# Performance work log

Measured on AMD Instinct MI355X. Metric: run time of the kernel, lower is better.

Reference implementation:

```python
import jax, jax.numpy as jnp
import numpy as np

MAX_ITERS = 30
NDIM = 3
TAU = 1.0 / (2.0 * NDIM)  # skimage Chambolle step size


def _grad(u, ax):
    # forward difference along ax, zero at the last slice (skimage convention)
    g = jnp.diff(u, axis=ax)
    pad = [(0, 0)] * u.ndim
    pad[ax] = (0, 1)
    return jnp.pad(g, pad)


def _div(p):
    # adjoint of _grad: d[ax] = shift_forward(p[ax]) - p[ax]
    d = jnp.zeros_like(p[0])
    for ax in range(NDIM):
        pa = p[ax]
        sl = [slice(None)] * NDIM
        sl[ax] = slice(0, -1)
        pad = [(0, 0)] * NDIM
        pad[ax] = (1, 0)
        d = d + jnp.pad(pa[tuple(sl)], pad) - pa
    return d


def tv_chambolle_nd(image, weight):
    # Chambolle projection algorithm (skimage _denoise_tv_chambolle_nd), fixed iters.
    def step(p, _):
        out = image + _div(p)
        g = jnp.stack([_grad(out, ax) for ax in range(NDIM)], axis=0)  # (3,B,T,F)
        norm = jnp.sqrt(jnp.sum(g * g, axis=0, keepdims=True))
        norm = norm * (TAU / weight) + 1.0
        return (p - TAU * g) / norm, None

    p0 = jnp.zeros((NDIM,) + image.shape, image.dtype)
    # iteration i returns out built from p after i updates; after max_iters loop
    # iterations the returned `out` used p updated (max_iters-1) times.
    p, _ = jax.lax.scan(jax.checkpoint(step), p0, None, length=MAX_ITERS - 1)
    return image + _div(p)


def setup_inputs() -> dict:
    key = jax.random.key(0)
    kx, kl, kb = jax.random.split(key, 3)
    x = jax.random.normal(kx, (8, 2048, 128), dtype=jnp.float32)
    # lambdas has a non-neg constraint; keep it strictly positive
    lambdas = jax.random.uniform(kl, (1, 1), dtype=jnp.float32) * 0.1 + 0.05
    b = jax.random.normal(kb, (1, 1, 128), dtype=jnp.float32) * 0.01
    return {"x": x, "lambdas": lambdas, "b": b}


def reference(x, lambdas, b):
    out = tv_chambolle_nd(x.astype(jnp.float32), lambdas)
    out = out + b  # use_bias=True; activation=None
    return out
```

## Files before the change

### kernel.cpp

```cpp
#include <hip/hip_runtime.h>
#include <hip/hip_fp16.h>


#define BB 8
#define TT 2048
#define FF 128
#define NV (BB*TT*FF)
#define SB (TT*FF)
#define ST FF
#define RR 8
#define NBLK (TT/RR)
#define HH 4
#define EE 16
#define GR 8

constexpr float TAU = 1.0f / 6.0f;

__device__ __forceinline__ float4 ld4(const float* p) { return *reinterpret_cast<const float4*>(p); }
__device__ __forceinline__ void st4(float* p, const float4& v) { *reinterpret_cast<float4*>(p) = v; }
__device__ __forceinline__ float4 ld4h(const __half* p) {
    uint2 u = *reinterpret_cast<const uint2*>(p);
    __half2 h0 = *reinterpret_cast<__half2*>(&u.x);
    __half2 h1 = *reinterpret_cast<__half2*>(&u.y);
    float2 a = __half22float2(h0), b2 = __half22float2(h1);
    return make_float4(a.x, a.y, b2.x, b2.y);
}
__device__ __forceinline__ void st4h(__half* p, const float4& v) {
    __half2 h0 = __float22half2_rn(make_float2(v.x, v.y));
    __half2 h1 = __float22half2_rn(make_float2(v.z, v.w));
    uint2 u;
    u.x = *reinterpret_cast<unsigned*>(&h0);
    u.y = *reinterpret_cast<unsigned*>(&h1);
    *reinterpret_cast<uint2*>(p) = u;
}
__device__ __forceinline__ float dpp_shr1(float v) {
    return __int_as_float(__builtin_amdgcn_update_dpp(
        0, __float_as_int(v), 0x111, 0xF, 0xF, true));
}
__device__ __forceinline__ float dpp_shl1(float v) {
    return __int_as_float(__builtin_amdgcn_update_dpp(
        0, __float_as_int(v), 0x101, 0xF, 0xF, true));
}
__device__ __forceinline__ float4 dpp_up4(const float4& v) {
    return make_float4(dpp_shr1(v.x), dpp_shr1(v.y), dpp_shr1(v.z), dpp_shr1(v.w));
}
__device__ __forceinline__ float4 dpp_dn4(const float4& v) {
    return make_float4(dpp_shl1(v.x), dpp_shl1(v.y), dpp_shl1(v.z), dpp_shl1(v.w));
}
__device__ __forceinline__ float4 sub4(const float4& a, const float4& b) {
    return make_float4(a.x - b.x, a.y - b.y, a.z - b.z, a.w - b.w);
}
__device__ __forceinline__ float4 f4z() { return make_float4(0.f, 0.f, 0.f, 0.f); }
__device__ __forceinline__ float4 nbvec(const float4& gB, const float4& gT, const float4& gF, float s) {
    float4 nb; float q;
    q = gB.x * gB.x + gT.x * gT.x + gF.x * gF.x;
    nb.x = __builtin_amdgcn_rcpf(fmaf(__builtin_amdgcn_sqrtf(q), s, 1.f));
    q = gB.y * gB.y + gT.y * gT.y + gF.y * gF.y;
    nb.y = __builtin_amdgcn_rcpf(fmaf(__builtin_amdgcn_sqrtf(q), s, 1.f));
    q = gB.z * gB.z + gT.z * gT.z + gF.z * gF.z;
    nb.z = __builtin_amdgcn_rcpf(fmaf(__builtin_amdgcn_sqrtf(q), s, 1.f));
    q = gB.w * gB.w + gT.w * gT.w + gF.w * gF.w;
    nb.w = __builtin_amdgcn_rcpf(fmaf(__builtin_amdgcn_sqrtf(q), s, 1.f));
    return nb;
}

struct ConeShared {
    float p2b[EE][4][8];
    float outx[EE][4][8];
    float4 p1if[256];
    float4 oif[256];
};

template<int RG>
__device__ __forceinline__ void publish(int k, float4 (&P1)[GR], float4 (&P2)[GR],
                                        ConeShared& sh, int c, int b, int fg, int w) {
    if (fg == 7) {
        #pragma unroll
        for (int le = 0; le < GR; ++le) {
            const int e = RG * GR + le;
            if (e >= k && e < EE - k) sh.p2b[e][w][b] = P2[le].w;
        }
    }
    if (RG == 0) sh.p1if[c] = P1[GR - 1];
}

template<int RG, bool ELO, bool EHI>
__device__ __forceinline__ void phase_out(
    int k, const float4 (&Xr)[GR],
    float4 (&P0)[GR], float4 (&P1)[GR], float4 (&P2)[GR], float4 (&O)[GR],
    ConeShared& sh, int c, int b, int fg, int w, int f0, int tb) {
    #pragma unroll
    for (int le = 0; le < GR; ++le) {
        const int e = RG * GR + le;
        if (e < k + 1 || e >= EE - k) continue;
        const int t = tb + e;
        if ((ELO && t < 0) || (EHI && t >= TT)) continue;
        const float4 X = Xr[le];
        float4 o;
        o.x = X.x - P0[le].x - P1[le].x - P2[le].x;
        o.y = X.y - P0[le].y - P1[le].y - P2[le].y + P2[le].x;
        o.z = X.z - P0[le].z - P1[le].z - P2[le].z + P2[le].y;
        o.w = X.w - P0[le].w - P1[le].w - P2[le].w + P2[le].z;
        float4 h0 = dpp_up4(P0[le]);
        if (b > 0) { o.x += h0.x; o.y += h0.y; o.z += h0.z; o.w += h0.w; }
        float4 pm1 = (le > 0) ? P1[le - 1] : sh.p1if[c];
        if (!ELO || t > 0) { o.x += pm1.x; o.y += pm1.y; o.z += pm1.z; o.w += pm1.w; }
        float pw = __shfl_up(P2[le].w, 8);
        if (fg == 0) pw = (w > 0) ? sh.p2b[e][(w - 1)][b] : 0.0f;
        if (f0 > 0) o.x += pw;
        O[le] = o;
        if (fg == 0) sh.outx[e][w][b] = o.x;
    }
}

template<int RG, bool ELO, bool EHI>
__device__ __forceinline__ void phase_upd(
    int k, float4 (&P0)[GR], float4 (&P1)[GR], float4 (&P2)[GR], float4 (&O)[GR],
    ConeShared& sh, int c, int b, int fg, int w, int f0, int tb, float s) {
    #pragma unroll
    for (int le = 0; le < GR; ++le) {
        const int e = RG * GR + le;
        if (e < k + 1 || e > EE - 2 - k) continue;
        const int t = tb + e;
        if ((ELO && t < 0) || (EHI && t >= TT)) continue;
        const float4 cc = O[le];
        const float4 on = (le < GR - 1) ? O[le + 1] : sh.oif[c];
        float4 gT = f4z();
        if (!EHI || t < TT - 1) gT = sub4(on, cc);
        const float4 nB = dpp_dn4(cc);
        float4 gB = f4z();
        if (b < BB - 1) gB = sub4(nB, cc);
        float nxx = __shfl_down(cc.x, 8);
        if (fg == 7) nxx = (w < 3) ? sh.outx[e][w + 1][b] : 0.0f;
        float4 gF;
        gF.x = cc.y - cc.x;
        gF.y = cc.z - cc.y;
        gF.z = cc.w - cc.z;
        gF.w = (f0 < FF - 4) ? (nxx - cc.w) : 0.f;
        const float4 nb = nbvec(gB, gT, gF, s);
        P0[le].x = fmaf(-TAU, gB.x, P0[le].x) * nb.x;
        P0[le].y = fmaf(-TAU, gB.y, P0[le].y) * nb.y;
        P0[le].z = fmaf(-TAU, gB.z, P0[le].z) * nb.z;
        P0[le].w = fmaf(-TAU, gB.w, P0[le].w) * nb.w;
        P1[le].x = fmaf(-TAU, gT.x, P1[le].x) * nb.x;
        P1[le].y = fmaf(-TAU, gT.y, P1[le].y) * nb.y;
        P1[le].z = fmaf(-TAU, gT.z, P1[le].z) * nb.z;
        P1[le].w = fmaf(-TAU, gT.w, P1[le].w) * nb.w;
        P2[le].x = fmaf(-TAU, gF.x, P2[le].x) * nb.x;
        P2[le].y = fmaf(-TAU, gF.y, P2[le].y) * nb.y;
        P2[le].z = fmaf(-TAU, gF.z, P2[le].z) * nb.z;
        P2[le].w = fmaf(-TAU, gF.w, P2[le].w) * nb.w;
    }
}

template<bool ELO, bool EHI>
__device__ __forceinline__ void cone_run(
    const float4 (&Xr)[GR],
    float4 (&P0)[GR], float4 (&P1)[GR], float4 (&P2)[GR], float4 (&O)[GR],
    ConeShared& sh, int rg, int c, int b, int fg, int w, int f0, int tb, float s) {
    #pragma unroll
    for (int k = 0; k < HH; ++k) {
        if (rg == 0) publish<0>(k, P1, P2, sh, c, b, fg, w);
        else         publish<1>(k, P1, P2, sh, c, b, fg, w);
        __syncthreads();
        if (rg == 0) phase_out<0, ELO, EHI>(k, Xr, P0, P1, P2, O, sh, c, b, fg, w, f0, tb);
        else         phase_out<1, ELO, EHI>(k, Xr, P0, P1, P2, O, sh, c, b, fg, w, f0, tb);
        if (rg == 1) sh.oif[c] = O[0];
        __syncthreads();
        if (rg == 0) phase_upd<0, ELO, EHI>(k, P0, P1, P2, O, sh, c, b, fg, w, f0, tb, s);
        else         phase_upd<1, ELO, EHI>(k, P0, P1, P2, O, sh, c, b, fg, w, f0, tb, s);
    }
}

template<bool ELO, bool EHI>
__device__ __forceinline__ void mid_main(
    const float* __restrict__ x, const __half* __restrict__ pin, __half* __restrict__ pout,
    ConeShared& sh, int rg, int c, int b, int fg, int w, int f0, int tb, int e0,
    int base, float s) {
    float4 P0[GR], P1[GR], P2[GR], O[GR], Xr[GR];
    #pragma unroll
    for (int le = 0; le < GR; ++le) {
        const int t = tb + e0 + le;
        const bool ok = (!ELO || t >= 0) && (!EHI || t < TT);
        const bool trim = (rg == 0 && le == 0);
        if (ok) {
            const int v = base + t * ST;
            P1[le] = ld4h(pin + NV + v);
            if (!trim) {
                P0[le] = ld4h(pin + v);
                P2[le] = ld4h(pin + 2 * NV + v);
                Xr[le] = ld4(x + v);
            } else { P0[le] = f4z(); P2[le] = f4z(); Xr[le] = f4z(); }
        } else {
            P0[le] = f4z(); P1[le] = f4z(); P2[le] = f4z(); Xr[le] = f4z();
        }
        O[le] = f4z();
    }
    cone_run<ELO, EHI>(Xr, P0, P1, P2, O, sh, rg, c, b, fg, w, f0, tb, s);
    #pragma unroll
    for (int le = 0; le < GR; ++le) {
        const int e = e0 + le;
        if (e >= HH && e < HH + RR) {
            const int v = base + (tb + e) * ST;
            st4h(pout + v, P0[le]);
            st4h(pout + NV + v, P1[le]);
            st4h(pout + 2 * NV + v, P2[le]);
        }
    }
}

__global__ __launch_bounds__(512, 2)
void k_mid(const float* __restrict__ x, const __half* __restrict__ pin,
           __half* __restrict__ pout, const float* __restrict__ lam) {
    __shared__ ConeShared sh;
    const int tid = threadIdx.x;
    const int blk = blockIdx.x;
    const int rg  = tid >> 8;
    const int c   = tid & 255;
    const int b   = tid & 7;
    const int fg  = (tid >> 3) & 7;
    const int w   = (tid >> 6) & 3;
    const int f0  = w * 32 + fg * 4;
    const int tb  = blk * RR - HH;
    const int e0  = rg * GR;
    const int base = b * SB + f0;
    const float s = TAU / lam[0];
    if (blk == 0 || blk == NBLK - 1)
        mid_main<true, true>(x, pin, pout, sh, rg, c, b, fg, w, f0, tb, e0, base, s);
    else
        mid_main<false, false>(x, pin, pout, sh, rg, c, b, fg, w, f0, tb, e0, base, s);
}

template<bool ELO, bool EHI>
__device__ __forceinline__ void first_main(
    const float* __restrict__ x, __half* __restrict__ pout,
    ConeShared& sh, int rg, int c, int b, int fg, int w, int f0, int tb, int e0,
    int base, float s) {
    float4 P0[GR], P1[GR], P2[GR], O[GR], Xr[GR], XHa;
    #pragma unroll
    for (int le = 0; le < GR; ++le) {
        const int t = tb + e0 + le;
        const bool ok = (!ELO || t >= 0) && (!EHI || t < TT);
        Xr[le] = ok ? ld4(x + base + t * ST) : f4z();
        O[le] = f4z();
    }
    {
        const int t = tb + e0 + GR;
        const bool ok = (!ELO || t >= 0) && (t < TT);
        XHa = ok ? ld4(x + base + t * ST) : f4z();
    }
    #pragma unroll
    for (int le = 0; le < GR; ++le) {
        const int t = tb + e0 + le;
        if ((!ELO || t >= 0) && (!EHI || t < TT)) {
            const float4 cc = Xr[le];
            const float4 nxt = (le < GR - 1) ? Xr[le + 1] : XHa;
            float4 gT = f4z();
            if (t < TT - 1) gT = sub4(nxt, cc);
            const float4 nB = dpp_dn4(cc);
            float4 gB = f4z();
            if (b < BB - 1) gB = sub4(nB, cc);
            float4 gF;
            gF.x = cc.y - cc.x;
            gF.y = cc.z - cc.y;
            gF.z = cc.w - cc.z;
            gF.w = (f0 < FF - 4) ? (x[base + t * ST + 4] - cc.w) : 0.f;
            const float4 nb = nbvec(gB, gT, gF, s);
            P0[le] = make_float4(-TAU * gB.x * nb.x, -TAU * gB.y * nb.y,
                                 -TAU * gB.z * nb.z, -TAU * gB.w * nb.w);
            P1[le] = make_float4(-TAU * gT.x * nb.x, -TAU * gT.y * nb.y,
                                 -TAU * gT.z * nb.z, -TAU * gT.w * nb.w);
            P2[le] = make_float4(-TAU * gF.x * nb.x, -TAU * gF.y * nb.y,
                                 -TAU * gF.z * nb.z, -TAU * gF.w * nb.w);
        } else {
            P0[le] = f4z(); P1[le] = f4z(); P2[le] = f4z();
        }
    }
    cone_run<ELO, EHI>(Xr, P0, P1, P2, O, sh, rg, c, b, fg, w, f0, tb, s);
    #pragma unroll
    for (int le = 0; le < GR; ++le) {
        const int e = e0 + le;
        if (e >= HH && e < HH + RR) {
            const int v = base + (tb + e) * ST;
            st4h(pout + v, P0[le]);
            st4h(pout + NV + v, P1[le]);
            st4h(pout + 2 * NV + v, P2[le]);
        }
    }
}

__global__ __launch_bounds__(512, 2)
void k_first(const float* __restrict__ x, __half* __restrict__ pout,
             const float* __restrict__ lam) {
    __shared__ ConeShared sh;
    const int tid = threadIdx.x;
    const int blk = blockIdx.x;
    const int rg  = tid >> 8;
    const int c   = tid & 255;
    const int b   = tid & 7;
    const int fg  = (tid >> 3) & 7;
    const int w   = (tid >> 6) & 3;
    const int f0  = w * 32 + fg * 4;
    const int tb  = blk * RR - HH;
    const int e0  = rg * GR;
    const int base = b * SB + f0;
    const float s = TAU / lam[0];
    if (blk == 0 || blk == NBLK - 1)
        first_main<true, true>(x, pout, sh, rg, c, b, fg, w, f0, tb, e0, base, s);
    else
        first_main<false, false>(x, pout, sh, rg, c, b, fg, w, f0, tb, e0, base, s);
}

__global__ __launch_bounds__(256)
void k_final(const float* __restrict__ x, const __half* __restrict__ pin,
             const float* __restrict__ bias, float* __restrict__ out) {
    const int gid = blockIdx.x * 256 + threadIdx.x;
    const int v = gid * 4;
    const int f0 = v & (FF - 1);
    const int t = (v >> 7) & (TT - 1);
    const int b = v >> 18;
    const __half* p0 = pin;
    const __half* p1 = pin + NV;
    const __half* p2 = pin + 2 * NV;
    float4 X = ld4(x + v);
    float4 a0 = ld4h(p0 + v), a1 = ld4h(p1 + v), a2 = ld4h(p2 + v);
    float ox = X.x - a0.x - a1.x - a2.x;
    float oy = X.y - a0.y - a1.y - a2.y + a2.x;
    float oz = X.z - a0.z - a1.z - a2.z + a2.y;
    float ow = X.w - a0.w - a1.w - a2.w + a2.z;
    if (b > 0) { float4 h = ld4h(p0 + v - SB); ox += h.x; oy += h.y; oz += h.z; ow += h.w; }
    if (t > 0) { float4 h = ld4h(p1 + v - ST); ox += h.x; oy += h.y; oz += h.z; ow += h.w; }
    if (f0 > 0) ox += __half2float(p2[v - 1]);
    float4 bi = ld4(bias + f0);
    st4(out + v, make_float4(ox + bi.x, oy + bi.y, oz + bi.z, ow + bi.w));
}

extern "C" void kernel_launch(void* const* d_in, const int* in_sizes, int n_in,
                              void* d_out, int out_size, void* d_ws, size_t ws_size,
                              hipStream_t stream) {
    const float* x    = (const float*)d_in[0];
    const float* lam  = (const float*)d_in[1];
    const float* bias = (const float*)d_in[2];
    float* out = (float*)d_out;

    __half* pA = (__half*)d_ws;
    __half* pB = pA + 3 * NV;

    k_first<<<NBLK, 512, 0, stream>>>(x, pA, lam);
    __half* pin = pA;
    __half* pout = pB;
    for (int i = 0; i < 6; ++i) {
        k_mid<<<NBLK, 512, 0, stream>>>(x, pin, pout, lam);
        __half* tmp = pin; pin = pout; pout = tmp;
    }
    k_final<<<NV / 1024, 256, 0, stream>>>(x, pin, bias, out);
}
```

Baseline: 245.7 us.

## Hold dual variables as packed half in registers and shrink temporal tiles

The per-thread dual arrays P0/P1/P2 become packed half (h4) in registers and are converted to float only for arithmetic. The time tile shrinks from 8 to 4 rows, with a 12-row cone and 6 rows per group, and launch bounds go to 4 blocks per CU. The aim is to cut VGPR pressure so more waves are resident. In exchange, halo recomputation grows with the smaller tile, many more blocks are launched, and dual values are now rounded to fp16 on every iteration inside a cone rather than only at global stores.

```diff
diff --git a/kernel.cpp b/kernel.cpp
--- a/kernel.cpp
+++ b/kernel.cpp
@@ -8,31 +8,49 @@
 #define NV (BB*TT*FF)
 #define SB (TT*FF)
 #define ST FF
-#define RR 8
+#define RR 4
 #define NBLK (TT/RR)
 #define HH 4
-#define EE 16
-#define GR 8
+#define EE 12
+#define GR 6
 
 constexpr float TAU = 1.0f / 6.0f;
 
 __device__ __forceinline__ float4 ld4(const float* p) { return *reinterpret_cast<const float4*>(p); }
 __device__ __forceinline__ void st4(float* p, const float4& v) { *reinterpret_cast<float4*>(p) = v; }
-__device__ __forceinline__ float4 ld4h(const __half* p) {
+
+struct h4 { __half2 lo, hi; };
+__device__ __forceinline__ float4 h2f(const h4& h) {
+    float2 a = __half22float2(h.lo), b = __half22float2(h.hi);
+    return make_float4(a.x, a.y, b.x, b.y);
+}
+__device__ __forceinline__ h4 f2h(const float4& v) {
+    h4 r;
+    r.lo = __float22half2_rn(make_float2(v.x, v.y));
+    r.hi = __float22half2_rn(make_float2(v.z, v.w));
+    return r;
+}
+__device__ __forceinline__ h4 h4z() {
+    h4 r; unsigned z = 0;
+    r.lo = *reinterpret_cast<__half2*>(&z);
+    r.hi = *reinterpret_cast<__half2*>(&z);
+    return r;
+}
+__device__ __forceinline__ h4 ld4hp(const __half* p) {
     uint2 u = *reinterpret_cast<const uint2*>(p);
-    __half2 h0 = *reinterpret_cast<__half2*>(&u.x);
-    __half2 h1 = *reinterpret_cast<__half2*>(&u.y);
-    float2 a = __half22float2(h0), b2 = __half22float2(h1);
-    return make_float4(a.x, a.y, b2.x, b2.y);
-}
-__device__ __forceinline__ void st4h(__half* p, const float4& v) {
-    __half2 h0 = __float22half2_rn(make_float2(v.x, v.y));
-    __half2 h1 = __float22half2_rn(make_float2(v.z, v.w));
+    h4 r;
+    r.lo = *reinterpret_cast<__half2*>(&u.x);
+    r.hi = *reinterpret_cast<__half2*>(&u.y);
+    return r;
+}
+__device__ __forceinline__ void st4hp(__half* p, const h4& v) {
     uint2 u;
-    u.x = *reinterpret_cast<unsigned*>(&h0);
-    u.y = *reinterpret_cast<unsigned*>(&h1);
+    u.x = *reinterpret_cast<const unsigned*>(&v.lo);
+    u.y = *reinterpret_cast<const unsigned*>(&v.hi);
     *reinterpret_cast<uint2*>(p) = u;
 }
+__device__ __forceinline__ float4 ld4h(const __half* p) { return h2f(ld4hp(p)); }
+
 __device__ __forceinline__ float dpp_shr1(float v) {
     return __int_as_float(__builtin_amdgcn_update_dpp(
         0, __float_as_int(v), 0x111, 0xF, 0xF, true));
@@ -41,11 +59,18 @@
     return __int_as_float(__builtin_amdgcn_update_dpp(
         0, __float_as_int(v), 0x101, 0xF, 0xF, true));
 }
-__device__ __forceinline__ float4 dpp_up4(const float4& v) {
-    return make_float4(dpp_shr1(v.x), dpp_shr1(v.y), dpp_shr1(v.z), dpp_shr1(v.w));
-}
 __device__ __forceinline__ float4 dpp_dn4(const float4& v) {
     return make_float4(dpp_shl1(v.x), dpp_shl1(v.y), dpp_shl1(v.z), dpp_shl1(v.w));
+}
+__device__ __forceinline__ h4 dpp_up_h4(const h4& v) {
+    unsigned lo = *reinterpret_cast<const unsigned*>(&v.lo);
+    unsigned hi = *reinterpret_cast<const unsigned*>(&v.hi);
+    unsigned rl = (unsigned)__builtin_amdgcn_update_dpp(0, (int)lo, 0x111, 0xF, 0xF, true);
+    unsigned rh = (unsigned)__builtin_amdgcn_update_dpp(0, (int)hi, 0x111, 0xF, 0xF, true);
+    h4 r;
+    r.lo = *reinterpret_cast<__half2*>(&rl);
+    r.hi = *reinterpret_cast<__half2*>(&rh);
+    return r;
 }
 __device__ __forceinline__ float4 sub4(const float4& a, const float4& b) {
     return make_float4(a.x - b.x, a.y - b.y, a.z - b.z, a.w - b.w);
@@ -67,18 +92,18 @@
 struct ConeShared {
     float p2b[EE][4][8];
     float outx[EE][4][8];
-    float4 p1if[256];
+    h4 p1if[256];
     float4 oif[256];
 };
 
 template<int RG>
-__device__ __forceinline__ void publish(int k, float4 (&P1)[GR], float4 (&P2)[GR],
+__device__ __forceinline__ void publish(int k, h4 (&P1)[GR], h4 (&P2)[GR],
                                         ConeShared& sh, int c, int b, int fg, int w) {
     if (fg == 7) {
         #pragma unroll
         for (int le = 0; le < GR; ++le) {
             const int e = RG * GR + le;
-            if (e >= k && e < EE - k) sh.p2b[e][w][b] = P2[le].w;
+            if (e >= k && e < EE - k) sh.p2b[e][w][b] = __high2float(P2[le].hi);
         }
     }
     if (RG == 0) sh.p1if[c] = P1[GR - 1];
@@ -87,7 +112,7 @@
 template<int RG, bool ELO, bool EHI>
 __device__ __forceinline__ void phase_out(
     int k, const float4 (&Xr)[GR],
-    float4 (&P0)[GR], float4 (&P1)[GR], float4 (&P2)[GR], float4 (&O)[GR],
+    h4 (&P0)[GR], h4 (&P1)[GR], h4 (&P2)[GR], float4 (&O)[GR],
     ConeShared& sh, int c, int b, int fg, int w, int f0, int tb) {
     #pragma unroll
     for (int le = 0; le < GR; ++le) {
@@ -96,16 +121,20 @@
         const int t = tb + e;
         if ((ELO && t < 0) || (EHI && t >= TT)) continue;
         const float4 X = Xr[le];
+        const float4 p0 = h2f(P0[le]);
+        const float4 p1 = h2f(P1[le]);
+        const float4 p2 = h2f(P2[le]);
         float4 o;
-        o.x = X.x - P0[le].x - P1[le].x - P2[le].x;
-        o.y = X.y - P0[le].y - P1[le].y - P2[le].y + P2[le].x;
-        o.z = X.z - P0[le].z - P1[le].z - P2[le].z + P2[le].y;
-        o.w = X.w - P0[le].w - P1[le].w - P2[le].w + P2[le].z;
-        float4 h0 = dpp_up4(P0[le]);
+        o.x = X.x - p0.x - p1.x - p2.x;
+        o.y = X.y - p0.y - p1.y - p2.y + p2.x;
+        o.z = X.z - p0.z - p1.z - p2.z + p2.y;
+        o.w = X.w - p0.w - p1.w - p2.w + p2.z;
+        const float4 h0 = h2f(dpp_up_h4(P0[le]));
         if (b > 0) { o.x += h0.x; o.y += h0.y; o.z += h0.z; o.w += h0.w; }
-        float4 pm1 = (le > 0) ? P1[le - 1] : sh.p1if[c];
+        const h4 pm1h = (le > 0) ? P1[le - 1] : sh.p1if[c];
+        const float4 pm1 = h2f(pm1h);
         if (!ELO || t > 0) { o.x += pm1.x; o.y += pm1.y; o.z += pm1.z; o.w += pm1.w; }
-        float pw = __shfl_up(P2[le].w, 8);
+        float pw = __shfl_up(p2.w, 8);
         if (fg == 0) pw = (w > 0) ? sh.p2b[e][(w - 1)][b] : 0.0f;
         if (f0 > 0) o.x += pw;
         O[le] = o;
@@ -115,7 +144,7 @@
 
 template<int RG, bool ELO, bool EHI>
 __device__ __forceinline__ void phase_upd(
-    int k, float4 (&P0)[GR], float4 (&P1)[GR], float4 (&P2)[GR], float4 (&O)[GR],
+    int k, h4 (&P0)[GR], h4 (&P1)[GR], h4 (&P2)[GR], float4 (&O)[GR],
     ConeShared& sh, int c, int b, int fg, int w, int f0, int tb, float s) {
     #pragma unroll
     for (int le = 0; le < GR; ++le) {
@@ -138,25 +167,32 @@
         gF.z = cc.w - cc.z;
         gF.w = (f0 < FF - 4) ? (nxx - cc.w) : 0.f;
         const float4 nb = nbvec(gB, gT, gF, s);
-        P0[le].x = fmaf(-TAU, gB.x, P0[le].x) * nb.x;
-        P0[le].y = fmaf(-TAU, gB.y, P0[le].y) * nb.y;
-        P0[le].z = fmaf(-TAU, gB.z, P0[le].z) * nb.z;
-        P0[le].w = fmaf(-TAU, gB.w, P0[le].w) * nb.w;
-        P1[le].x = fmaf(-TAU, gT.x, P1[le].x) * nb.x;
-        P1[le].y = fmaf(-TAU, gT.y, P1[le].y) * nb.y;
-        P1[le].z = fmaf(-TAU, gT.z, P1[le].z) * nb.z;
-        P1[le].w = fmaf(-TAU, gT.w, P1[le].w) * nb.w;
-        P2[le].x = fmaf(-TAU, gF.x, P2[le].x) * nb.x;
-        P2[le].y = fmaf(-TAU, gF.y, P2[le].y) * nb.y;
-        P2[le].z = fmaf(-TAU, gF.z, P2[le].z) * nb.z;
-        P2[le].w = fmaf(-TAU, gF.w, P2[le].w) * nb.w;
+        const float4 p0 = h2f(P0[le]);
+        const float4 p1 = h2f(P1[le]);
+        const float4 p2 = h2f(P2[le]);
+        float4 n0, n1, n2;
+        n0.x = fmaf(-TAU, gB.x, p0.x) * nb.x;
+        n0.y = fmaf(-TAU, gB.y, p0.y) * nb.y;
+        n0.z = fmaf(-TAU, gB.z, p0.z) * nb.z;
+        n0.w = fmaf(-TAU, gB.w, p0.w) * nb.w;
+        n1.x = fmaf(-TAU, gT.x, p1.x) * nb.x;
+        n1.y = fmaf(-TAU, gT.y, p1.y) * nb.y;
+        n1.z = fmaf(-TAU, gT.z, p1.z) * nb.z;
+        n1.w = fmaf(-TAU, gT.w, p1.w) * nb.w;
+        n2.x = fmaf(-TAU, gF.x, p2.x) * nb.x;
+        n2.y = fmaf(-TAU, gF.y, p2.y) * nb.y;
+        n2.z = fmaf(-TAU, gF.z, p2.z) * nb.z;
+        n2.w = fmaf(-TAU, gF.w, p2.w) * nb.w;
+        P0[le] = f2h(n0);
+        P1[le] = f2h(n1);
+        P2[le] = f2h(n2);
     }
 }
 
 template<bool ELO, bool EHI>
 __device__ __forceinline__ void cone_run(
     const float4 (&Xr)[GR],
-    float4 (&P0)[GR], float4 (&P1)[GR], float4 (&P2)[GR], float4 (&O)[GR],
+    h4 (&P0)[GR], h4 (&P1)[GR], h4 (&P2)[GR], float4 (&O)[GR],
     ConeShared& sh, int rg, int c, int b, int fg, int w, int f0, int tb, float s) {
     #pragma unroll
     for (int k = 0; k < HH; ++k) {
@@ -177,7 +213,8 @@
     const float* __restrict__ x, const __half* __restrict__ pin, __half* __restrict__ pout,
     ConeShared& sh, int rg, int c, int b, int fg, int w, int f0, int tb, int e0,
     int base, float s) {
-    float4 P0[GR], P1[GR], P2[GR], O[GR], Xr[GR];
+    h4 P0[GR], P1[GR], P2[GR];
+    float4 O[GR], Xr[GR];
     #pragma unroll
     for (int le = 0; le < GR; ++le) {
         const int t = tb + e0 + le;
@@ -185,14 +222,14 @@
         const bool trim = (rg == 0 && le == 0);
         if (ok) {
             const int v = base + t * ST;
-            P1[le] = ld4h(pin + NV + v);
+            P1[le] = ld4hp(pin + NV + v);
             if (!trim) {
-                P0[le] = ld4h(pin + v);
-                P2[le] = ld4h(pin + 2 * NV + v);
+                P0[le] = ld4hp(pin + v);
+                P2[le] = ld4hp(pin + 2 * NV + v);
                 Xr[le] = ld4(x + v);
-            } else { P0[le] = f4z(); P2[le] = f4z(); Xr[le] = f4z(); }
+            } else { P0[le] = h4z(); P2[le] = h4z(); Xr[le] = f4z(); }
         } else {
-            P0[le] = f4z(); P1[le] = f4z(); P2[le] = f4z(); Xr[le] = f4z();
+            P0[le] = h4z(); P1[le] = h4z(); P2[le] = h4z(); Xr[le] = f4z();
         }
         O[le] = f4z();
     }
@@ -202,14 +239,14 @@
         const int e = e0 + le;
         if (e >= HH && e < HH + RR) {
             const int v = base + (tb + e) * ST;
-            st4h(pout + v, P0[le]);
-            st4h(pout + NV + v, P1[le]);
-            st4h(pout + 2 * NV + v, P2[le]);
-        }
-    }
-}
-
-__global__ __launch_bounds__(512, 2)
+            st4hp(pout + v, P0[le]);
+            st4hp(pout + NV + v, P1[le]);
+            st4hp(pout + 2 * NV + v, P2[le]);
+        }
+    }
+}
+
+__global__ __launch_bounds__(512, 4)
 void k_mid(const float* __restrict__ x, const __half* __restrict__ pin,
            __half* __restrict__ pout, const float* __restrict__ lam) {
     __shared__ ConeShared sh;
@@ -236,7 +273,8 @@
     const float* __restrict__ x, __half* __restrict__ pout,
     ConeShared& sh, int rg, int c, int b, int fg, int w, int f0, int tb, int e0,
     int base, float s) {
-    float4 P0[GR], P1[GR], P2[GR], O[GR], Xr[GR], XHa;
+    h4 P0[GR], P1[GR], P2[GR];
+    float4 O[GR], Xr[GR], XHa;
     #pragma unroll
     for (int le = 0; le < GR; ++le) {
         const int t = tb + e0 + le;
@@ -266,14 +304,14 @@
             gF.z = cc.w - cc.z;
             gF.w = (f0 < FF - 4) ? (x[base + t * ST + 4] - cc.w) : 0.f;
             const float4 nb = nbvec(gB, gT, gF, s);
-            P0[le] = make_float4(-TAU * gB.x * nb.x, -TAU * gB.y * nb.y,
-                                 -TAU * gB.z * nb.z, -TAU * gB.w * nb.w);
-            P1[le] = make_float4(-TAU * gT.x * nb.x, -TAU * gT.y * nb.y,
-                                 -TAU * gT.z * nb.z, -TAU * gT.w * nb.w);
-            P2[le] = make_float4(-TAU * gF.x * nb.x, -TAU * gF.y * nb.y,
-                                 -TAU * gF.z * nb.z, -TAU * gF.w * nb.w);
+            P0[le] = f2h(make_float4(-TAU * gB.x * nb.x, -TAU * gB.y * nb.y,
+                                     -TAU * gB.z * nb.z, -TAU * gB.w * nb.w));
+            P1[le] = f2h(make_float4(-TAU * gT.x * nb.x, -TAU * gT.y * nb.y,
+                                     -TAU * gT.z * nb.z, -TAU * gT.w * nb.w));
+            P2[le] = f2h(make_float4(-TAU * gF.x * nb.x, -TAU * gF.y * nb.y,
+                                     -TAU * gF.z * nb.z, -TAU * gF.w * nb.w));
         } else {
-            P0[le] = f4z(); P1[le] = f4z(); P2[le] = f4z();
+            P0[le] = h4z(); P1[le] = h4z(); P2[le] = h4z();
         }
     }
     cone_run<ELO, EHI>(Xr, P0, P1, P2, O, sh, rg, c, b, fg, w, f0, tb, s);
@@ -282,14 +320,14 @@
         const int e = e0 + le;
         if (e >= HH && e < HH + RR) {
             const int v = base + (tb + e) * ST;
-            st4h(pout + v, P0[le]);
-            st4h(pout + NV + v, P1[le]);
-            st4h(pout + 2 * NV + v, P2[le]);
-        }
-    }
-}
-
-__global__ __launch_bounds__(512, 2)
+            st4hp(pout + v, P0[le]);
+            st4hp(pout + NV + v, P1[le]);
+            st4hp(pout + 2 * NV + v, P2[le]);
+        }
+    }
+}
+
+__global__ __launch_bounds__(512, 4)
 void k_first(const float* __restrict__ x, __half* __restrict__ pout,
              const float* __restrict__ lam) {
     __shared__ ConeShared sh;
```

After: 438.8 us. +78.6%, slower.

## Fuse all phases into one persistent cooperative kernel with grid syncs

Applied to the files above, without the earlier changes.

Replaces the first, six middle and final kernel launches with a single cooperative persistent kernel. Each block keeps its x slice and interior p state in registers across phases and reloads only the halo rows from global memory after each grid-wide sync. The final output is computed in registers with a last publish and sync step. This removes launch gaps and repeated interior loads and stores, at the cost of grid-sync overhead and the requirement that all 256 blocks be co-resident.

```diff
diff --git a/kernel.cpp b/kernel.cpp
--- a/kernel.cpp
+++ b/kernel.cpp
@@ -1,5 +1,8 @@
 #include <hip/hip_runtime.h>
 #include <hip/hip_fp16.h>
+#include <hip/hip_cooperative_groups.h>
+
+namespace cg = cooperative_groups;
 
 
 #define BB 8
@@ -173,67 +176,9 @@
 }
 
 template<bool ELO, bool EHI>
-__device__ __forceinline__ void mid_main(
-    const float* __restrict__ x, const __half* __restrict__ pin, __half* __restrict__ pout,
-    ConeShared& sh, int rg, int c, int b, int fg, int w, int f0, int tb, int e0,
-    int base, float s) {
-    float4 P0[GR], P1[GR], P2[GR], O[GR], Xr[GR];
-    #pragma unroll
-    for (int le = 0; le < GR; ++le) {
-        const int t = tb + e0 + le;
-        const bool ok = (!ELO || t >= 0) && (!EHI || t < TT);
-        const bool trim = (rg == 0 && le == 0);
-        if (ok) {
-            const int v = base + t * ST;
-            P1[le] = ld4h(pin + NV + v);
-            if (!trim) {
-                P0[le] = ld4h(pin + v);
-                P2[le] = ld4h(pin + 2 * NV + v);
-                Xr[le] = ld4(x + v);
-            } else { P0[le] = f4z(); P2[le] = f4z(); Xr[le] = f4z(); }
-        } else {
-            P0[le] = f4z(); P1[le] = f4z(); P2[le] = f4z(); Xr[le] = f4z();
-        }
-        O[le] = f4z();
-    }
-    cone_run<ELO, EHI>(Xr, P0, P1, P2, O, sh, rg, c, b, fg, w, f0, tb, s);
-    #pragma unroll
-    for (int le = 0; le < GR; ++le) {
-        const int e = e0 + le;
-        if (e >= HH && e < HH + RR) {
-            const int v = base + (tb + e) * ST;
-            st4h(pout + v, P0[le]);
-            st4h(pout + NV + v, P1[le]);
-            st4h(pout + 2 * NV + v, P2[le]);
-        }
-    }
-}
-
-__global__ __launch_bounds__(512, 2)
-void k_mid(const float* __restrict__ x, const __half* __restrict__ pin,
-           __half* __restrict__ pout, const float* __restrict__ lam) {
-    __shared__ ConeShared sh;
-    const int tid = threadIdx.x;
-    const int blk = blockIdx.x;
-    const int rg  = tid >> 8;
-    const int c   = tid & 255;
-    const int b   = tid & 7;
-    const int fg  = (tid >> 3) & 7;
-    const int w   = (tid >> 6) & 3;
-    const int f0  = w * 32 + fg * 4;
-    const int tb  = blk * RR - HH;
-    const int e0  = rg * GR;
-    const int base = b * SB + f0;
-    const float s = TAU / lam[0];
-    if (blk == 0 || blk == NBLK - 1)
-        mid_main<true, true>(x, pin, pout, sh, rg, c, b, fg, w, f0, tb, e0, base, s);
-    else
-        mid_main<false, false>(x, pin, pout, sh, rg, c, b, fg, w, f0, tb, e0, base, s);
-}
-
-template<bool ELO, bool EHI>
-__device__ __forceinline__ void first_main(
-    const float* __restrict__ x, __half* __restrict__ pout,
+__device__ __forceinline__ void persist_main(
+    const float* __restrict__ x, __half* __restrict__ pA, __half* __restrict__ pB,
+    const float* __restrict__ bias, float* __restrict__ out,
     ConeShared& sh, int rg, int c, int b, int fg, int w, int f0, int tb, int e0,
     int base, float s) {
     float4 P0[GR], P1[GR], P2[GR], O[GR], Xr[GR], XHa;
@@ -277,21 +222,72 @@
         }
     }
     cone_run<ELO, EHI>(Xr, P0, P1, P2, O, sh, rg, c, b, fg, w, f0, tb, s);
+    for (int ph = 0; ph < 6; ++ph) {
+        __half* buf = (ph & 1) ? pB : pA;
+        #pragma unroll
+        for (int le = 0; le < GR; ++le) {
+            const int e = e0 + le;
+            if (e >= HH && e < HH + RR) {
+                const int v = base + (tb + e) * ST;
+                st4h(buf + v, P0[le]);
+                st4h(buf + NV + v, P1[le]);
+                st4h(buf + 2 * NV + v, P2[le]);
+            }
+        }
+        __threadfence();
+        cg::this_grid().sync();
+        #pragma unroll
+        for (int le = 0; le < GR; ++le) {
+            const bool halo = (rg == 0) ? (le < HH) : (le >= GR - HH);
+            if (halo) {
+                const int t = tb + e0 + le;
+                const bool ok = (!ELO || t >= 0) && (!EHI || t < TT);
+                const bool trim = (rg == 0 && le == 0);
+                if (ok) {
+                    const int v = base + t * ST;
+                    P1[le] = ld4h(buf + NV + v);
+                    if (!trim) {
+                        P0[le] = ld4h(buf + v);
+                        P2[le] = ld4h(buf + 2 * NV + v);
+                    } else { P0[le] = f4z(); P2[le] = f4z(); }
+                } else {
+                    P0[le] = f4z(); P1[le] = f4z(); P2[le] = f4z();
+                }
+            }
+        }
+        cone_run<ELO, EHI>(Xr, P0, P1, P2, O, sh, rg, c, b, fg, w, f0, tb, s);
+    }
+    if (rg == 1) {
+        const int t = tb + HH + RR - 1;
+        st4h(pA + NV + base + t * ST, P1[HH + RR - 1 - GR]);
+    }
+    if (rg == 0) publish<0>(HH, P1, P2, sh, c, b, fg, w);
+    else         publish<1>(HH, P1, P2, sh, c, b, fg, w);
+    __threadfence();
+    cg::this_grid().sync();
+    if (rg == 0) {
+        const int t = tb + HH - 1;
+        if (!ELO || t >= 0) P1[HH - 1] = ld4h(pA + NV + base + t * ST);
+    }
+    if (rg == 0) phase_out<0, ELO, EHI>(HH - 1, Xr, P0, P1, P2, O, sh, c, b, fg, w, f0, tb);
+    else         phase_out<1, ELO, EHI>(HH - 1, Xr, P0, P1, P2, O, sh, c, b, fg, w, f0, tb);
+    const float4 bi = ld4(bias + f0);
     #pragma unroll
     for (int le = 0; le < GR; ++le) {
         const int e = e0 + le;
         if (e >= HH && e < HH + RR) {
-            const int v = base + (tb + e) * ST;
-            st4h(pout + v, P0[le]);
-            st4h(pout + NV + v, P1[le]);
-            st4h(pout + 2 * NV + v, P2[le]);
+            const int t = tb + e;
+            const float4 o = O[le];
+            st4(out + base + t * ST,
+                make_float4(o.x + bi.x, o.y + bi.y, o.z + bi.z, o.w + bi.w));
         }
     }
 }
 
 __global__ __launch_bounds__(512, 2)
-void k_first(const float* __restrict__ x, __half* __restrict__ pout,
-             const float* __restrict__ lam) {
+void k_persist(const float* __restrict__ x, __half* __restrict__ pA,
+               __half* __restrict__ pB, const float* __restrict__ lam,
+               const float* __restrict__ bias, float* __restrict__ out) {
     __shared__ ConeShared sh;
     const int tid = threadIdx.x;
     const int blk = blockIdx.x;
@@ -306,33 +302,9 @@
     const int base = b * SB + f0;
     const float s = TAU / lam[0];
     if (blk == 0 || blk == NBLK - 1)
-        first_main<true, true>(x, pout, sh, rg, c, b, fg, w, f0, tb, e0, base, s);
+        persist_main<true, true>(x, pA, pB, bias, out, sh, rg, c, b, fg, w, f0, tb, e0, base, s);
     else
-        first_main<false, false>(x, pout, sh, rg, c, b, fg, w, f0, tb, e0, base, s);
-}
-
-__global__ __launch_bounds__(256)
-void k_final(const float* __restrict__ x, const __half* __restrict__ pin,
-             const float* __restrict__ bias, float* __restrict__ out) {
-    const int gid = blockIdx.x * 256 + threadIdx.x;
-    const int v = gid * 4;
-    const int f0 = v & (FF - 1);
-    const int t = (v >> 7) & (TT - 1);
-    const int b = v >> 18;
-    const __half* p0 = pin;
-    const __half* p1 = pin + NV;
-    const __half* p2 = pin + 2 * NV;
-    float4 X = ld4(x + v);
-    float4 a0 = ld4h(p0 + v), a1 = ld4h(p1 + v), a2 = ld4h(p2 + v);
-    float ox = X.x - a0.x - a1.x - a2.x;
-    float oy = X.y - a0.y - a1.y - a2.y + a2.x;
-    float oz = X.z - a0.z - a1.z - a2.z + a2.y;
-    float ow = X.w - a0.w - a1.w - a2.w + a2.z;
-    if (b > 0) { float4 h = ld4h(p0 + v - SB); ox += h.x; oy += h.y; oz += h.z; ow += h.w; }
-    if (t > 0) { float4 h = ld4h(p1 + v - ST); ox += h.x; oy += h.y; oz += h.z; ow += h.w; }
-    if (f0 > 0) ox += __half2float(p2[v - 1]);
-    float4 bi = ld4(bias + f0);
-    st4(out + v, make_float4(ox + bi.x, oy + bi.y, oz + bi.z, ow + bi.w));
+        persist_main<false, false>(x, pA, pB, bias, out, sh, rg, c, b, fg, w, f0, tb, e0, base, s);
 }
 
 extern "C" void kernel_launch(void* const* d_in, const int* in_sizes, int n_in,
@@ -346,12 +318,8 @@
     __half* pA = (__half*)d_ws;
     __half* pB = pA + 3 * NV;
 
-    k_first<<<NBLK, 512, 0, stream>>>(x, pA, lam);
-    __half* pin = pA;
-    __half* pout = pB;
-    for (int i = 0; i < 6; ++i) {
-        k_mid<<<NBLK, 512, 0, stream>>>(x, pin, pout, lam);
-        __half* tmp = pin; pin = pout; pout = tmp;
-    }
-    k_final<<<NV / 1024, 256, 0, stream>>>(x, pin, bias, out);
-}
+    void* args[] = {(void*)&x, (void*)&pA, (void*)&pB,
+                    (void*)&lam, (void*)&bias, (void*)&out};
+    hipLaunchCooperativeKernel((void*)k_persist, dim3(NBLK), dim3(512),
+                               args, 0, stream);
+}
```

Measured after the change: 958.5 us. +290.1%, slower.

## Fuse last temporal-blocked iteration group with final divergence and bias output

Applied to the files above, without the earlier changes.

Replaces the standalone final divergence kernel with a tail kernel that runs four Chambolle iterations in a halo-extended time cone (18 rows, halo 5) and then computes the output plus bias directly. One mid launch is dropped, removing a full round trip of the fp16 dual field through global memory and one launch. The tail keeps p in half-precision registers and adds redundant halo computation and extra shared-memory exchanges.

```diff
diff --git a/kernel.cpp b/kernel.cpp
--- a/kernel.cpp
+++ b/kernel.cpp
@@ -13,6 +13,9 @@
 #define HH 4
 #define EE 16
 #define GR 8
+#define EET 18
+#define GRT 9
+#define HLT 5
 
 constexpr float TAU = 1.0f / 6.0f;
 
@@ -33,6 +36,31 @@
     u.y = *reinterpret_cast<unsigned*>(&h1);
     *reinterpret_cast<uint2*>(p) = u;
 }
+struct h4 { __half2 lo, hi; };
+__device__ __forceinline__ float4 h2f(const h4& h) {
+    float2 a = __half22float2(h.lo), b = __half22float2(h.hi);
+    return make_float4(a.x, a.y, b.x, b.y);
+}
+__device__ __forceinline__ h4 f2h(const float4& v) {
+    h4 r;
+    r.lo = __float22half2_rn(make_float2(v.x, v.y));
+    r.hi = __float22half2_rn(make_float2(v.z, v.w));
+    return r;
+}
+__device__ __forceinline__ h4 h4z() {
+    h4 r; unsigned z = 0;
+    r.lo = *reinterpret_cast<__half2*>(&z);
+    r.hi = *reinterpret_cast<__half2*>(&z);
+    return r;
+}
+__device__ __forceinline__ h4 ld4hp(const __half* p) {
+    uint2 u = *reinterpret_cast<const uint2*>(p);
+    h4 r;
+    r.lo = *reinterpret_cast<__half2*>(&u.x);
+    r.hi = *reinterpret_cast<__half2*>(&u.y);
+    return r;
+}
+
 __device__ __forceinline__ float dpp_shr1(float v) {
     return __int_as_float(__builtin_amdgcn_update_dpp(
         0, __float_as_int(v), 0x111, 0xF, 0xF, true));
@@ -46,6 +74,16 @@
 }
 __device__ __forceinline__ float4 dpp_dn4(const float4& v) {
     return make_float4(dpp_shl1(v.x), dpp_shl1(v.y), dpp_shl1(v.z), dpp_shl1(v.w));
+}
+__device__ __forceinline__ h4 dpp_up_h4(const h4& v) {
+    unsigned lo = *reinterpret_cast<const unsigned*>(&v.lo);
+    unsigned hi = *reinterpret_cast<const unsigned*>(&v.hi);
+    unsigned rl = (unsigned)__builtin_amdgcn_update_dpp(0, (int)lo, 0x111, 0xF, 0xF, true);
+    unsigned rh = (unsigned)__builtin_amdgcn_update_dpp(0, (int)hi, 0x111, 0xF, 0xF, true);
+    h4 r;
+    r.lo = *reinterpret_cast<__half2*>(&rl);
+    r.hi = *reinterpret_cast<__half2*>(&rh);
+    return r;
 }
 __device__ __forceinline__ float4 sub4(const float4& a, const float4& b) {
     return make_float4(a.x - b.x, a.y - b.y, a.z - b.z, a.w - b.w);
@@ -311,28 +349,184 @@
         first_main<false, false>(x, pout, sh, rg, c, b, fg, w, f0, tb, e0, base, s);
 }
 
-__global__ __launch_bounds__(256)
-void k_final(const float* __restrict__ x, const __half* __restrict__ pin,
-             const float* __restrict__ bias, float* __restrict__ out) {
-    const int gid = blockIdx.x * 256 + threadIdx.x;
-    const int v = gid * 4;
-    const int f0 = v & (FF - 1);
-    const int t = (v >> 7) & (TT - 1);
-    const int b = v >> 18;
-    const __half* p0 = pin;
-    const __half* p1 = pin + NV;
-    const __half* p2 = pin + 2 * NV;
-    float4 X = ld4(x + v);
-    float4 a0 = ld4h(p0 + v), a1 = ld4h(p1 + v), a2 = ld4h(p2 + v);
-    float ox = X.x - a0.x - a1.x - a2.x;
-    float oy = X.y - a0.y - a1.y - a2.y + a2.x;
-    float oz = X.z - a0.z - a1.z - a2.z + a2.y;
-    float ow = X.w - a0.w - a1.w - a2.w + a2.z;
-    if (b > 0) { float4 h = ld4h(p0 + v - SB); ox += h.x; oy += h.y; oz += h.z; ow += h.w; }
-    if (t > 0) { float4 h = ld4h(p1 + v - ST); ox += h.x; oy += h.y; oz += h.z; ow += h.w; }
-    if (f0 > 0) ox += __half2float(p2[v - 1]);
-    float4 bi = ld4(bias + f0);
-    st4(out + v, make_float4(ox + bi.x, oy + bi.y, oz + bi.z, ow + bi.w));
+struct ConeSharedT {
+    float p2b[EET][4][8];
+    float outx[EET][4][8];
+    h4 p1if[256];
+    float4 oif[256];
+};
+
+template<int RG>
+__device__ __forceinline__ void publish_t(int k, h4 (&P1)[GRT], h4 (&P2)[GRT],
+                                          ConeSharedT& sh, int c, int b, int fg, int w) {
+    if (fg == 7) {
+        #pragma unroll
+        for (int le = 0; le < GRT; ++le) {
+            const int e = RG * GRT + le;
+            if (e >= k && e < EET - k) sh.p2b[e][w][b] = __high2float(P2[le].hi);
+        }
+    }
+    if (RG == 0) sh.p1if[c] = P1[GRT - 1];
+}
+
+template<int RG, bool ELO, bool EHI>
+__device__ __forceinline__ void phase_out_t(
+    int k, const float4 (&Xr)[GRT],
+    h4 (&P0)[GRT], h4 (&P1)[GRT], h4 (&P2)[GRT], float4 (&O)[GRT],
+    ConeSharedT& sh, int c, int b, int fg, int w, int f0, int tb) {
+    #pragma unroll
+    for (int le = 0; le < GRT; ++le) {
+        const int e = RG * GRT + le;
+        if (e < k + 1 || e >= EET - k) continue;
+        const int t = tb + e;
+        if ((ELO && t < 0) || (EHI && t >= TT)) continue;
+        const float4 X = Xr[le];
+        const float4 p0 = h2f(P0[le]);
+        const float4 p1 = h2f(P1[le]);
+        const float4 p2 = h2f(P2[le]);
+        float4 o;
+        o.x = X.x - p0.x - p1.x - p2.x;
+        o.y = X.y - p0.y - p1.y - p2.y + p2.x;
+        o.z = X.z - p0.z - p1.z - p2.z + p2.y;
+        o.w = X.w - p0.w - p1.w - p2.w + p2.z;
+        const float4 h0 = h2f(dpp_up_h4(P0[le]));
+        if (b > 0) { o.x += h0.x; o.y += h0.y; o.z += h0.z; o.w += h0.w; }
+        const h4 pm1h = (le > 0) ? P1[le - 1] : sh.p1if[c];
+        const float4 pm1 = h2f(pm1h);
+        if (!ELO || t > 0) { o.x += pm1.x; o.y += pm1.y; o.z += pm1.z; o.w += pm1.w; }
+        float pw = __shfl_up(p2.w, 8);
+        if (fg == 0) pw = (w > 0) ? sh.p2b[e][(w - 1)][b] : 0.0f;
+        if (f0 > 0) o.x += pw;
+        O[le] = o;
+        if (fg == 0) sh.outx[e][w][b] = o.x;
+    }
+}
+
+template<int RG, bool ELO, bool EHI>
+__device__ __forceinline__ void phase_upd_t(
+    int k, h4 (&P0)[GRT], h4 (&P1)[GRT], h4 (&P2)[GRT], float4 (&O)[GRT],
+    ConeSharedT& sh, int c, int b, int fg, int w, int f0, int tb, float s) {
+    #pragma unroll
+    for (int le = 0; le < GRT; ++le) {
+        const int e = RG * GRT + le;
+        if (e < k + 1 || e > EET - 2 - k) continue;
+        const int t = tb + e;
+        if ((ELO && t < 0) || (EHI && t >= TT)) continue;
+        const float4 cc = O[le];
+        const float4 on = (le < GRT - 1) ? O[le + 1] : sh.oif[c];
+        float4 gT = f4z();
+        if (!EHI || t < TT - 1) gT = sub4(on, cc);
+        const float4 nB = dpp_dn4(cc);
+        float4 gB = f4z();
+        if (b < BB - 1) gB = sub4(nB, cc);
+        float nxx = __shfl_down(cc.x, 8);
+        if (fg == 7) nxx = (w < 3) ? sh.outx[e][w + 1][b] : 0.0f;
+        float4 gF;
+        gF.x = cc.y - cc.x;
+        gF.y = cc.z - cc.y;
+        gF.z = cc.w - cc.z;
+        gF.w = (f0 < FF - 4) ? (nxx - cc.w) : 0.f;
+        const float4 nb = nbvec(gB, gT, gF, s);
+        const float4 p0 = h2f(P0[le]);
+        const float4 p1 = h2f(P1[le]);
+        const float4 p2 = h2f(P2[le]);
+        float4 n0, n1, n2;
+        n0.x = fmaf(-TAU, gB.x, p0.x) * nb.x;
+        n0.y = fmaf(-TAU, gB.y, p0.y) * nb.y;
+        n0.z = fmaf(-TAU, gB.z, p0.z) * nb.z;
+        n0.w = fmaf(-TAU, gB.w, p0.w) * nb.w;
+        n1.x = fmaf(-TAU, gT.x, p1.x) * nb.x;
+        n1.y = fmaf(-TAU, gT.y, p1.y) * nb.y;
+        n1.z = fmaf(-TAU, gT.z, p1.z) * nb.z;
+        n1.w = fmaf(-TAU, gT.w, p1.w) * nb.w;
+        n2.x = fmaf(-TAU, gF.x, p2.x) * nb.x;
+        n2.y = fmaf(-TAU, gF.y, p2.y) * nb.y;
+        n2.z = fmaf(-TAU, gF.z, p2.z) * nb.z;
+        n2.w = fmaf(-TAU, gF.w, p2.w) * nb.w;
+        P0[le] = f2h(n0);
+        P1[le] = f2h(n1);
+        P2[le] = f2h(n2);
+    }
+}
+
+template<bool ELO, bool EHI>
+__device__ __forceinline__ void tail_main(
+    const float* __restrict__ x, const __half* __restrict__ pin,
+    const float* __restrict__ bias, float* __restrict__ out,
+    ConeSharedT& sh, int rg, int c, int b, int fg, int w, int f0, int tb, int e0,
+    int base, float s) {
+    h4 P0[GRT], P1[GRT], P2[GRT];
+    float4 O[GRT], Xr[GRT];
+    #pragma unroll
+    for (int le = 0; le < GRT; ++le) {
+        const int t = tb + e0 + le;
+        const bool ok = (!ELO || t >= 0) && (!EHI || t < TT);
+        const bool trim = (rg == 0 && le == 0);
+        if (ok) {
+            const int v = base + t * ST;
+            P1[le] = ld4hp(pin + NV + v);
+            if (!trim) {
+                P0[le] = ld4hp(pin + v);
+                P2[le] = ld4hp(pin + 2 * NV + v);
+                Xr[le] = ld4(x + v);
+            } else { P0[le] = h4z(); P2[le] = h4z(); Xr[le] = f4z(); }
+        } else {
+            P0[le] = h4z(); P1[le] = h4z(); P2[le] = h4z(); Xr[le] = f4z();
+        }
+        O[le] = f4z();
+    }
+    #pragma unroll
+    for (int k = 0; k < 4; ++k) {
+        if (rg == 0) publish_t<0>(k, P1, P2, sh, c, b, fg, w);
+        else         publish_t<1>(k, P1, P2, sh, c, b, fg, w);
+        __syncthreads();
+        if (rg == 0) phase_out_t<0, ELO, EHI>(k, Xr, P0, P1, P2, O, sh, c, b, fg, w, f0, tb);
+        else         phase_out_t<1, ELO, EHI>(k, Xr, P0, P1, P2, O, sh, c, b, fg, w, f0, tb);
+        if (rg == 1) sh.oif[c] = O[0];
+        __syncthreads();
+        if (rg == 0) phase_upd_t<0, ELO, EHI>(k, P0, P1, P2, O, sh, c, b, fg, w, f0, tb, s);
+        else         phase_upd_t<1, ELO, EHI>(k, P0, P1, P2, O, sh, c, b, fg, w, f0, tb, s);
+    }
+    __syncthreads();
+    if (rg == 0) publish_t<0>(4, P1, P2, sh, c, b, fg, w);
+    else         publish_t<1>(4, P1, P2, sh, c, b, fg, w);
+    __syncthreads();
+    if (rg == 0) phase_out_t<0, ELO, EHI>(4, Xr, P0, P1, P2, O, sh, c, b, fg, w, f0, tb);
+    else         phase_out_t<1, ELO, EHI>(4, Xr, P0, P1, P2, O, sh, c, b, fg, w, f0, tb);
+    const float4 bi = ld4(bias + f0);
+    #pragma unroll
+    for (int le = 0; le < GRT; ++le) {
+        const int e = e0 + le;
+        if (e >= HLT && e < HLT + RR) {
+            const int t = tb + e;
+            const float4 o = O[le];
+            st4(out + base + t * ST,
+                make_float4(o.x + bi.x, o.y + bi.y, o.z + bi.z, o.w + bi.w));
+        }
+    }
+}
+
+__global__ __launch_bounds__(512, 2)
+void k_tail(const float* __restrict__ x, const __half* __restrict__ pin,
+            const float* __restrict__ lam, const float* __restrict__ bias,
+            float* __restrict__ out) {
+    __shared__ ConeSharedT sh;
+    const int tid = threadIdx.x;
+    const int blk = blockIdx.x;
+    const int rg  = tid >> 8;
+    const int c   = tid & 255;
+    const int b   = tid & 7;
+    const int fg  = (tid >> 3) & 7;
+    const int w   = (tid >> 6) & 3;
+    const int f0  = w * 32 + fg * 4;
+    const int tb  = blk * RR - HLT;
+    const int e0  = rg * GRT;
+    const int base = b * SB + f0;
+    const float s = TAU / lam[0];
+    if (blk == 0 || blk == NBLK - 1)
+        tail_main<true, true>(x, pin, bias, out, sh, rg, c, b, fg, w, f0, tb, e0, base, s);
+    else
+        tail_main<false, false>(x, pin, bias, out, sh, rg, c, b, fg, w, f0, tb, e0, base, s);
 }
 
 extern "C" void kernel_launch(void* const* d_in, const int* in_sizes, int n_in,
@@ -349,9 +543,9 @@
     k_first<<<NBLK, 512, 0, stream>>>(x, pA, lam);
     __half* pin = pA;
     __half* pout = pB;
-    for (int i = 0; i < 6; ++i) {
+    for (int i = 0; i < 5; ++i) {
         k_mid<<<NBLK, 512, 0, stream>>>(x, pin, pout, lam);
         __half* tmp = pin; pin = pout; pout = tmp;
     }
-    k_final<<<NV / 1024, 256, 0, stream>>>(x, pin, bias, out);
-}
+    k_tail<<<NBLK, 512, 0, stream>>>(x, pin, lam, bias, out);
+}
```

New measurement: 245.6 us, median of 2. About the same (-0.0%).
